# Kernel optimization log

Hardware: AMD Instinct MI355X
Metric: run time of the kernel (lower is better)

The kernel has to match this reference:

```python
import jax, jax.numpy as jnp
import numpy as np

N = 50000      # num_nodes
E = 800000     # num_edges
C = 2000       # num_communities
F_NODE = 26    # n_demographic + 12
F_EDGE = 8     # num_edge_features
DEM = 14       # n_demographic
EMB = 64       # n_embedding
H2 = 2 * EMB   # 2*n_embedding == mask dim
HID = 128      # n_hidden (== H2 so the per-edge mask applies to both convs)


def setup_inputs() -> dict:
    key = jax.random.key(0)
    ks = jax.random.split(key, 40)
    def W(i, shape):
        return jax.random.normal(ks[i], shape, jnp.float32) * 0.05
    z = lambda d: jnp.zeros((d,), jnp.float32)
    return {
        "x": jax.random.normal(ks[0], (N, F_NODE), jnp.float32),
        "edge_attr": jax.random.uniform(ks[1], (E, F_EDGE), dtype=jnp.float32),
        "W_ee": W(2, (F_EDGE, EMB)), "b_ee": z(EMB),
        "W_e1": W(3, (DEM, EMB)), "b_e1": z(EMB),
        "W_e2": W(4, (12, EMB)), "b_e2": z(EMB),
        "W_e3": W(5, (H2, H2)), "b_e3": z(H2),
        "W_src": W(6, (H2, H2)), "W_dst": W(7, (H2, H2)), "W_ea": W(8, (EMB, H2)), "b_el": z(H2),
        "W_m": W(9, (H2, H2)), "b_m": z(H2),
        "W_n1": W(10, (H2, HID)), "W_r1": W(11, (H2, HID)), "b_c1": z(HID),
        "W_n2": W(12, (HID, HID)), "W_r2": W(13, (HID, HID)), "b_c2": z(HID),
        "W_l1": W(14, (2 * HID, HID)), "b_l1": z(HID),
        "W_l2": W(15, (HID, 1)), "b_l2": z(1),
        "edge_index": jax.random.randint(ks[16], (2, E), 0, N),
        "community": jax.random.randint(ks[17], (N,), 0, C),
        "multi_community_nodes": jax.random.randint(ks[18], (1000,), 0, N),
        "multi_community_index": jax.random.randint(ks[19], (1000,), 0, C),
    }


def _pool(h, community):
    # scatter_mean + scatter_max over communities, concatenated: [C, 2*d]
    sums = jax.ops.segment_sum(h, community, num_segments=C)
    cnt = jax.ops.segment_sum(jnp.ones((h.shape[0], 1), h.dtype), community, num_segments=C)
    mean = sums / jnp.maximum(cnt, 1.0)
    mx = jax.ops.segment_max(h, community, num_segments=C)
    mx = jnp.where(jnp.isfinite(mx), mx, 0.0)  # empty segments -> 0 (torch_scatter fill)
    return jnp.concatenate([mean, mx], axis=1)


def reference(x, edge_attr, W_ee, b_ee, W_e1, b_e1, W_e2, b_e2, W_e3, b_e3,
              W_src, W_dst, W_ea, b_el, W_m, b_m,
              W_n1, W_r1, b_c1, W_n2, W_r2, b_c2,
              W_l1, b_l1, W_l2, b_l2,
              edge_index, community, multi_community_nodes, multi_community_index):
    src, dst = edge_index[0], edge_index[1]
    # edge + node embeddings
    e = jax.nn.relu(edge_attr @ W_ee + b_ee)                      # [E, EMB]
    x1 = jax.nn.relu(x[:, :DEM] @ W_e1 + b_e1)                    # [N, EMB]
    x2 = jax.nn.relu(x[:, DEM:] @ W_e2 + b_e2)                    # [N, EMB]
    h = jax.nn.relu(jnp.concatenate([x1, x2], axis=1) @ W_e3 + b_e3)  # [N, H2]
    # edge learning: per-edge soft mask from endpoint features + edge embedding
    he = jax.nn.relu(h[src] @ W_src + h[dst] @ W_dst + e @ W_ea + b_el)  # [E, H2]
    mask = jax.nn.sigmoid(he @ W_m + b_m)                          # [E, H2]
    # mean-normalized masked message passing (ELConv)
    deg = jax.ops.segment_sum(jnp.ones((E, 1), h.dtype), dst, num_segments=N)
    deg_inv = 1.0 / jnp.maximum(deg, 1.0)                          # [N, 1]
    agg1 = jax.ops.segment_sum(h[src] * mask, dst, num_segments=N) * deg_inv
    h1 = jax.nn.relu(agg1 @ W_n1 + h @ W_r1 + b_c1)                # [N, HID]
    p1 = _pool(h1, community)                                      # [C, 2*HID]
    agg2 = jax.ops.segment_sum(h1[src] * mask, dst, num_segments=N) * deg_inv
    h2 = jax.nn.relu(agg2 @ W_n2 + h1 @ W_r2 + b_c2)               # [N, HID]
    p2 = _pool(h2, community)                                      # [C, 2*HID]
    p = p1 + p2
    out = jax.nn.relu(p @ W_l1 + b_l1)  # dropout skipped (eval mode)
    return (out @ W_l2 + b_l2)[:, 0]    # [C]
```

## Files before the change

### kernel.cpp

```cpp
#include <hip/hip_runtime.h>
#include <cstdint>
#include <cstddef>

#define kN 50000
#define kE 800000
#define kC 2000

using s8v = __attribute__((ext_vector_type(8))) short;
using s4v = __attribute__((ext_vector_type(4))) short;
using f4v = __attribute__((ext_vector_type(4))) float;

__device__ __forceinline__ short f2bf(float x){
  union { float f; unsigned u; } v; v.f = x;
  unsigned r = (v.u + 0x7fffu + ((v.u >> 16) & 1u)) >> 16;
  return (short)r;
}
__device__ __forceinline__ float bf2f(short s){
  union { unsigned u; float f; } v; v.u = ((unsigned)(unsigned short)s) << 16;
  return v.f;
}

__global__ __launch_bounds__(256) void k_hist(const int* __restrict__ dst, int* __restrict__ deg,
                                              const int* __restrict__ community, int* __restrict__ ccnt){
  int i = blockIdx.x*256 + threadIdx.x;
  if (i < kE) atomicAdd(&deg[dst[i]], 1);
  if (i < kN) atomicAdd(&ccnt[community[i]], 1);
}

__global__ __launch_bounds__(1024) void k_scan(const int* __restrict__ deg, int* __restrict__ offs){
  __shared__ int s_wsum[16];
  __shared__ int s_woff[17];
  __shared__ int s_carry;
  int t = threadIdx.x, lane = t & 63, w = t >> 6;
  if (t == 0) s_carry = 0;
  __syncthreads();
  for (int base = 0; base < kN; base += 4096){
    int i = base + t*4;
    int4 v = {0,0,0,0};
    if (i < kN) v = *reinterpret_cast<const int4*>(&deg[i]);
    int s = v.x + v.y + v.z + v.w;
    int x = s;
    #pragma unroll
    for (int off = 1; off < 64; off <<= 1){
      int y = __shfl_up(x, off);
      if (lane >= off) x += y;
    }
    if (lane == 63) s_wsum[w] = x;
    __syncthreads();
    if (t == 0){
      int acc = 0;
      for (int q = 0; q < 16; q++){ s_woff[q] = acc; acc += s_wsum[q]; }
      s_woff[16] = acc;
    }
    __syncthreads();
    if (i < kN){
      int pre = s_carry + s_woff[w] + (x - s);
      int4 o; o.x = pre; o.y = pre + v.x; o.z = pre + v.x + v.y; o.w = pre + v.x + v.y + v.z;
      *reinterpret_cast<int4*>(&offs[i]) = o;
    }
    __syncthreads();
    if (t == 0) s_carry += s_woff[16];
    __syncthreads();
  }
  if (t == 0) offs[kN] = s_carry;
}

__global__ __launch_bounds__(512) void k_scan_c(const int* __restrict__ ccnt, int* __restrict__ coffs){
  __shared__ int s_wsum[8];
  __shared__ int s_woff[9];
  int t = threadIdx.x, lane = t & 63, w = t >> 6;
  int i = t*4;
  int4 v = {0,0,0,0};
  if (i < kC) v = *reinterpret_cast<const int4*>(&ccnt[i]);
  int s = v.x + v.y + v.z + v.w;
  int x = s;
  #pragma unroll
  for (int off = 1; off < 64; off <<= 1){
    int y = __shfl_up(x, off);
    if (lane >= off) x += y;
  }
  if (lane == 63) s_wsum[w] = x;
  __syncthreads();
  if (t == 0){
    int a = 0;
    for (int q = 0; q < 8; q++){ s_woff[q] = a; a += s_wsum[q]; }
    s_woff[8] = a;
  }
  __syncthreads();
  if (i < kC){
    int pre = s_woff[w] + (x - s);
    int4 o; o.x = pre; o.y = pre + v.x; o.z = pre + v.x + v.y; o.w = pre + v.x + v.y + v.z;
    *reinterpret_cast<int4*>(&coffs[i]) = o;
  }
  if (t == 0) coffs[kC] = s_woff[8];
}

__global__ __launch_bounds__(256) void k_place(const int* __restrict__ src, const int* __restrict__ dst,
                                               const int* __restrict__ offs, int* __restrict__ cursor,
                                               int* __restrict__ pos_of_edge, int* __restrict__ src_sorted){
  int e = blockIdx.x*256 + threadIdx.x;
  if (e >= kE) return;
  int d = dst[e];
  int p = offs[d] + atomicAdd(&cursor[d], 1);
  pos_of_edge[e] = p;
  src_sorted[p]  = src[e];
}

__global__ __launch_bounds__(256) void k_place_c(const int* __restrict__ community, const int* __restrict__ coffs,
                                                 int* __restrict__ ccursor, int* __restrict__ node_by_comm){
  int n = blockIdx.x*256 + threadIdx.x;
  if (n >= kN) return;
  int c = community[n];
  int p = coffs[c] + atomicAdd(&ccursor[c], 1);
  node_by_comm[p] = n;
}

__global__ __launch_bounds__(512, 2) void k_embed_ab(
    const float* __restrict__ x,
    const float* __restrict__ W_e1, const float* __restrict__ b_e1,
    const float* __restrict__ W_e2, const float* __restrict__ b_e2,
    const float* __restrict__ W_e3, const float* __restrict__ b_e3,
    const float* __restrict__ W_src, const float* __restrict__ W_dst, const float* __restrict__ b_el,
    short* __restrict__ Hout, short* __restrict__ Aout, short* __restrict__ Bout, int ntiles)
{
  __shared__ short s_W[2][128][136];
  __shared__ float s_x[64][28];
  __shared__ float s_b3[128], s_bel[128];
  int tid = threadIdx.x;
  int lane = tid & 63, w = tid >> 6, lo = lane & 15, hi = lane >> 4;
  for (int idx = tid; idx < 128*128; idx += 512){
    int f = idx & 127, k = idx >> 7;
    s_W[0][f][k] = f2bf(W_e3[k*128 + f]);
    s_W[1][f][k] = f2bf(W_src[k*128 + f]);
  }
  if (tid < 128){ s_b3[tid] = b_e3[tid]; s_bel[tid] = b_el[tid]; }
  __syncthreads();
  s8v fe3[4], fsrc[4], fdst[4];
  #pragma unroll
  for (int ks = 0; ks < 4; ks++){
    fe3[ks]  = *(const s8v*)&s_W[0][w*16 + lo][ks*32 + hi*8];
    fsrc[ks] = *(const s8v*)&s_W[1][w*16 + lo][ks*32 + hi*8];
  }
  __syncthreads();
  for (int idx = tid; idx < 128*128; idx += 512){
    int f = idx & 127, k = idx >> 7;
    s_W[0][f][k] = f2bf(W_dst[k*128 + f]);
  }
  __syncthreads();
  #pragma unroll
  for (int ks = 0; ks < 4; ks++) fdst[ks] = *(const s8v*)&s_W[0][w*16 + lo][ks*32 + hi*8];

  short (*s_xe)[136] = s_W[0];
  short (*s_h)[136]  = s_W[1];

  for (int tile = blockIdx.x; tile < ntiles; tile += gridDim.x){
    int n0 = tile << 6;
    __syncthreads();
    for (int idx = tid; idx < 64*26; idx += 512){
      int nl = idx / 26, i = idx - nl*26; int n = n0 + nl;
      s_x[nl][i] = (n < kN) ? x[(size_t)n*26 + i] : 0.f;
    }
    __syncthreads();
    #pragma unroll
    for (int r = 0; r < 16; r++){
      int idx = (r << 9) + tid; int nl = idx >> 7, j = idx & 127;
      float a;
      if (j < 64){
        a = b_e1[j];
        #pragma unroll
        for (int i = 0; i < 14; i++) a += s_x[nl][i] * W_e1[i*64 + j];
      } else {
        int jj = j - 64;
        a = b_e2[jj];
        #pragma unroll
        for (int i = 0; i < 12; i++) a += s_x[nl][14 + i] * W_e2[i*64 + jj];
      }
      s_xe[nl][j] = f2bf(fmaxf(a, 0.f));
    }
    __syncthreads();
    #pragma unroll
    for (int et = 0; et < 4; et++){
      f4v acc = {0.f,0.f,0.f,0.f};
      #pragma unroll
      for (int ks = 0; ks < 4; ks++){
        s8v b = *(const s8v*)&s_xe[et*16 + lo][ks*32 + hi*8];
        acc = __builtin_amdgcn_mfma_f32_16x16x32_bf16(fe3[ks], b, acc, 0, 0, 0);
      }
      int n = n0 + et*16 + lo, f0 = w*16 + hi*4;
      s4v hv;
      #pragma unroll
      for (int j = 0; j < 4; j++) hv[j] = f2bf(fmaxf(acc[j] + s_b3[f0 + j], 0.f));
      *(s4v*)&s_h[et*16 + lo][f0] = hv;
      if (n < kN) *(s4v*)&Hout[(size_t)n*128 + f0] = hv;
    }
    __syncthreads();
    #pragma unroll
    for (int et = 0; et < 4; et++){
      f4v aA = {0.f,0.f,0.f,0.f}, aB = {0.f,0.f,0.f,0.f};
      #pragma unroll
      for (int ks = 0; ks < 4; ks++){
        s8v b = *(const s8v*)&s_h[et*16 + lo][ks*32 + hi*8];
        aA = __builtin_amdgcn_mfma_f32_16x16x32_bf16(fsrc[ks], b, aA, 0, 0, 0);
        aB = __builtin_amdgcn_mfma_f32_16x16x32_bf16(fdst[ks], b, aB, 0, 0, 0);
      }
      int n = n0 + et*16 + lo, f0 = w*16 + hi*4;
      if (n < kN){
        s4v Av, Bv;
        #pragma unroll
        for (int j = 0; j < 4; j++){ Av[j] = f2bf(aA[j] + s_bel[f0 + j]); Bv[j] = f2bf(aB[j]); }
        *(s4v*)&Aout[(size_t)n*128 + f0] = Av;
        *(s4v*)&Bout[(size_t)n*128 + f0] = Bv;
      }
    }
  }
}

#define OFF_WEA  0
#define OFF_WM   18432
#define OFF_EEMB 0
#define OFF_HE   9216
#define OFF_BIAS 26624
#define OFF_EA   59648
#define OFF_WEE  61696
#define OFF_BEE  63744
#define OFF_BM   64000
#define OFF_SRC  64512
#define OFF_DST  64768
#define OFF_POS  65024
__global__ __launch_bounds__(512, 4) void k_edge(
    const short* __restrict__ Abf, const short* __restrict__ Bbf,
    const float* __restrict__ edge_attr,
    const int* __restrict__ src, const int* __restrict__ dst,
    const int* __restrict__ posp,
    const float* __restrict__ W_ee, const float* __restrict__ b_ee,
    const float* __restrict__ W_ea, const float* __restrict__ W_m,
    const float* __restrict__ b_m,
    unsigned char* __restrict__ mask_out,
    int ntiles)
{
  __shared__ __align__(16) char smem[65280];
  short (*s_WeaT)[72]  = (short(*)[72])(smem + OFF_WEA);
  short (*s_WmT)[136]  = (short(*)[136])(smem + OFF_WM);
  short (*s_eemb)[72]  = (short(*)[72])(smem + OFF_EEMB);
  short (*s_he)[136]   = (short(*)[136])(smem + OFF_HE);
  float (*s_bias)[129] = (float(*)[129])(smem + OFF_BIAS);
  float (*s_ea)[8]     = (float(*)[8])(smem + OFF_EA);
  float *s_Wee = (float*)(smem + OFF_WEE);
  float *s_bee = (float*)(smem + OFF_BEE);
  float *s_bm  = (float*)(smem + OFF_BM);
  int *s_src = (int*)(smem + OFF_SRC);
  int *s_dst = (int*)(smem + OFF_DST);
  int *s_pos = (int*)(smem + OFF_POS);

  int tid = threadIdx.x;
  for (int idx = tid; idx < 128*64; idx += 512){ int f = idx & 127, k = idx >> 7; s_WeaT[f][k] = f2bf(W_ea[k*128+f]); }
  for (int idx = tid; idx < 128*128; idx += 512){ int f = idx & 127, k = idx >> 7; s_WmT[f][k] = f2bf(W_m[k*128+f]); }
  s_Wee[tid] = W_ee[tid];
  if (tid < 64) s_bee[tid] = b_ee[tid];
  if (tid >= 64 && tid < 192) s_bm[tid-64] = b_m[tid-64];
  __syncthreads();
  const int lane = tid & 63, w = tid >> 6;
  const int lo = lane & 15, hi = lane >> 4;
  const int el8 = tid >> 3, kb = (tid & 7) << 3;
  s8v a1[2], a2[4];
  #pragma unroll
  for (int ks = 0; ks < 2; ks++) a1[ks] = *(const s8v*)&s_WeaT[16*w + lo][ks*32 + hi*8];
  #pragma unroll
  for (int ks = 0; ks < 4; ks++) a2[ks] = *(const s8v*)&s_WmT[16*w + lo][ks*32 + hi*8];
  __syncthreads();

  for (int tile = blockIdx.x; tile < ntiles; tile += gridDim.x){
    int e0 = tile << 6;
    {
      int el = tid >> 3, i = tid & 7;
      s_ea[el][i] = edge_attr[(size_t)(e0 + el)*8 + i];
      if (tid < 192){
        int q = tid >> 6, r = tid & 63; int ee = e0 + r;
        if (q == 0)      s_src[r] = src[ee];
        else if (q == 1) s_dst[r] = dst[ee];
        else             s_pos[r] = posp[ee];
      }
    }
    __syncthreads();
    {
      int e = el8, part = tid & 7;
      int sb = s_src[e]*128 + part*16;
      int db = s_dst[e]*128 + part*16;
      s8v av0 = *(const s8v*)(Abf + sb);
      s8v av1 = *(const s8v*)(Abf + sb + 8);
      s8v bv0 = *(const s8v*)(Bbf + db);
      s8v bv1 = *(const s8v*)(Bbf + db + 8);
      float ee_[8];
      #pragma unroll
      for (int j = 0; j < 8; j++){
        float acc = s_bee[kb + j];
        #pragma unroll
        for (int i = 0; i < 8; i++) acc += s_ea[e][i] * s_Wee[i*64 + kb + j];
        ee_[j] = fmaxf(acc, 0.f);
      }
      s8v ep;
      #pragma unroll
      for (int j = 0; j < 8; j++) ep[j] = f2bf(ee_[j]);
      *(s8v*)&s_eemb[e][kb] = ep;
      #pragma unroll
      for (int q = 0; q < 8; q++){
        s_bias[e][part*16 + q]     = bf2f(av0[q]) + bf2f(bv0[q]);
        s_bias[e][part*16 + 8 + q] = bf2f(av1[q]) + bf2f(bv1[q]);
      }
    }
    __syncthreads();
    #pragma unroll
    for (int et = 0; et < 4; et++){
      f4v acc = {0.f, 0.f, 0.f, 0.f};
      #pragma unroll
      for (int ks = 0; ks < 2; ks++){
        s8v bfrag = *(const s8v*)&s_eemb[et*16 + lo][ks*32 + hi*8];
        acc = __builtin_amdgcn_mfma_f32_16x16x32_bf16(a1[ks], bfrag, acc, 0, 0, 0);
      }
      int e = et*16 + lo, f0 = 16*w + hi*4;
      s4v hw;
      #pragma unroll
      for (int j = 0; j < 4; j++) hw[j] = f2bf(fmaxf(acc[j] + s_bias[e][f0 + j], 0.f));
      *(s4v*)&s_he[e][f0] = hw;
    }
    __syncthreads();
    #pragma unroll
    for (int et = 0; et < 4; et++){
      f4v acc = {0.f, 0.f, 0.f, 0.f};
      #pragma unroll
      for (int ks = 0; ks < 4; ks++){
        s8v bfrag = *(const s8v*)&s_he[et*16 + lo][ks*32 + hi*8];
        acc = __builtin_amdgcn_mfma_f32_16x16x32_bf16(a2[ks], bfrag, acc, 0, 0, 0);
      }
      int e = et*16 + lo, f0 = 16*w + hi*4;
      unsigned pk = 0;
      #pragma unroll
      for (int j = 0; j < 4; j++){
        float m = 1.f/(1.f + __expf(-(acc[j] + s_bm[f0 + j])));
        pk |= (__float2uint_rn(m*255.f) & 255u) << (j*8);
      }
      *reinterpret_cast<unsigned*>(&mask_out[(size_t)s_pos[e]*128 + f0]) = pk;
    }
    __syncthreads();
  }
}

__global__ __launch_bounds__(512, 8) void k_conv(
    const short* __restrict__ Hbf,
    const unsigned char* __restrict__ mask8,
    const int* __restrict__ src_sorted, const int* __restrict__ offs,
    const float* __restrict__ Wn, const float* __restrict__ Wr, const float* __restrict__ bc,
    short* __restrict__ Hout, float* __restrict__ Pout, int ntiles)
{
  __shared__ short s_buf[128][136];
  __shared__ float s_bc[128];
  int tid = threadIdx.x;
  int lane = tid & 63, w = tid >> 6, lo = lane & 15, hi = lane >> 4;
  s8v fn[4], fr[4];
  for (int idx = tid; idx < 128*128; idx += 512){
    int f = idx & 127, k = idx >> 7;
    s_buf[f][k] = f2bf(Wn[k*128 + f]);
  }
  if (tid < 128) s_bc[tid] = bc[tid];
  __syncthreads();
  #pragma unroll
  for (int ks = 0; ks < 4; ks++) fn[ks] = *(const s8v*)&s_buf[w*16 + lo][ks*32 + hi*8];
  __syncthreads();
  for (int idx = tid; idx < 128*128; idx += 512){
    int f = idx & 127, k = idx >> 7;
    s_buf[f][k] = f2bf(Wr[k*128 + f]);
  }
  __syncthreads();
  #pragma unroll
  for (int ks = 0; ks < 4; ks++) fr[ks] = *(const s8v*)&s_buf[w*16 + lo][ks*32 + hi*8];

  short (*s_agg)[136] = s_buf;
  short (*s_h)[136]   = s_buf + 64;
  const int nl8 = tid >> 3, p16 = (tid & 7) << 4;

  for (int tile = blockIdx.x; tile < ntiles; tile += gridDim.x){
    int n0 = tile << 6;
    __syncthreads();
    int n = n0 + nl8;
    {
      s8v h0 = {0,0,0,0,0,0,0,0}, h1 = {0,0,0,0,0,0,0,0};
      if (n < kN){
        h0 = *(const s8v*)&Hbf[(size_t)n*128 + p16];
        h1 = *(const s8v*)&Hbf[(size_t)n*128 + p16 + 8];
      }
      *(s8v*)&s_h[nl8][p16] = h0;
      *(s8v*)&s_h[nl8][p16 + 8] = h1;
    }
    float acc[16];
    #pragma unroll
    for (int q = 0; q < 16; q++) acc[q] = 0.f;
    int s0 = 0, s1 = 0;
    if (n < kN){ s0 = offs[n]; s1 = offs[n+1]; }
    int4 mv_c = {0,0,0,0}; s8v g0_c = {0,0,0,0,0,0,0,0}, g1_c = {0,0,0,0,0,0,0,0};
    if (s0 < s1){
      int sv = src_sorted[s0];
      mv_c = *reinterpret_cast<const int4*>(&mask8[(size_t)s0*128 + p16]);
      g0_c = *(const s8v*)&Hbf[(size_t)sv*128 + p16];
      g1_c = *(const s8v*)&Hbf[(size_t)sv*128 + p16 + 8];
    }
    for (int i = s0; i < s1; i++){
      int4 mv = mv_c; s8v g0 = g0_c, g1 = g1_c;
      if (i + 1 < s1){
        int svn = src_sorted[i + 1];
        mv_c = *reinterpret_cast<const int4*>(&mask8[(size_t)(i+1)*128 + p16]);
        g0_c = *(const s8v*)&Hbf[(size_t)svn*128 + p16];
        g1_c = *(const s8v*)&Hbf[(size_t)svn*128 + p16 + 8];
      }
      unsigned mw[4] = {(unsigned)mv.x, (unsigned)mv.y, (unsigned)mv.z, (unsigned)mv.w};
      float mf[16];
      #pragma unroll
      for (int d = 0; d < 4; d++){
        mf[d*4+0] = (float)( mw[d]        & 255u);
        mf[d*4+1] = (float)((mw[d] >>  8) & 255u);
        mf[d*4+2] = (float)((mw[d] >> 16) & 255u);
        mf[d*4+3] = (float)( mw[d] >> 24       );
      }
      #pragma unroll
      for (int q = 0; q < 8; q++) acc[q]     += bf2f(g0[q]) * mf[q];
      #pragma unroll
      for (int q = 0; q < 8; q++) acc[8 + q] += bf2f(g1[q]) * mf[8 + q];
    }
    float inv = (1.f/255.f) / fmaxf((float)(s1 - s0), 1.f);
    {
      s8v a0, a1;
      #pragma unroll
      for (int q = 0; q < 8; q++){ a0[q] = f2bf(acc[q]*inv); a1[q] = f2bf(acc[8+q]*inv); }
      *(s8v*)&s_agg[nl8][p16] = a0;
      *(s8v*)&s_agg[nl8][p16 + 8] = a1;
    }
    __syncthreads();
    #pragma unroll
    for (int et = 0; et < 4; et++){
      f4v ac = {0.f,0.f,0.f,0.f};
      #pragma unroll
      for (int ks = 0; ks < 4; ks++){
        s8v bA = *(const s8v*)&s_agg[et*16 + lo][ks*32 + hi*8];
        ac = __builtin_amdgcn_mfma_f32_16x16x32_bf16(fn[ks], bA, ac, 0, 0, 0);
        s8v bH = *(const s8v*)&s_h[et*16 + lo][ks*32 + hi*8];
        ac = __builtin_amdgcn_mfma_f32_16x16x32_bf16(fr[ks], bH, ac, 0, 0, 0);
      }
      int nn = n0 + et*16 + lo, f0 = w*16 + hi*4;
      if (nn < kN){
        s4v hv; float4 pv;
        float v0 = fmaxf(ac[0] + s_bc[f0 + 0], 0.f);
        float v1 = fmaxf(ac[1] + s_bc[f0 + 1], 0.f);
        float v2 = fmaxf(ac[2] + s_bc[f0 + 2], 0.f);
        float v3 = fmaxf(ac[3] + s_bc[f0 + 3], 0.f);
        hv[0] = f2bf(v0); hv[1] = f2bf(v1); hv[2] = f2bf(v2); hv[3] = f2bf(v3);
        pv.x = v0; pv.y = v1; pv.z = v2; pv.w = v3;
        if (Hout) *(s4v*)&Hout[(size_t)nn*128 + f0] = hv;
        *reinterpret_cast<float4*>(&Pout[(size_t)nn*128 + f0]) = pv;
      }
    }
  }
}

__global__ __launch_bounds__(128) void k_final(
    const float* __restrict__ p1f, const float* __restrict__ p2f,
    const int* __restrict__ node_by_comm, const int* __restrict__ coffs,
    const float* __restrict__ W_l1, const float* __restrict__ b_l1,
    const float* __restrict__ W_l2, const float* __restrict__ b_l2,
    float* __restrict__ out)
{
  __shared__ float p[256];
  __shared__ float red[2];
  int c = blockIdx.x, t = threadIdx.x;
  int c0 = coffs[c], c1 = coffs[c+1];
  float s = 0.f, m1 = 0.f, m2 = 0.f;
  float v1_c = 0.f, v2_c = 0.f;
  if (c0 < c1){
    int n = node_by_comm[c0];
    v1_c = p1f[(size_t)n*128 + t];
    v2_c = p2f[(size_t)n*128 + t];
  }
  for (int i = c0; i < c1; i++){
    float v1 = v1_c, v2 = v2_c;
    if (i + 1 < c1){
      int nn = node_by_comm[i + 1];
      v1_c = p1f[(size_t)nn*128 + t];
      v2_c = p2f[(size_t)nn*128 + t];
    }
    s += v1 + v2;
    m1 = fmaxf(m1, v1);
    m2 = fmaxf(m2, v2);
  }
  float inv = 1.f / fmaxf((float)(c1 - c0), 1.f);
  p[t]       = s * inv;
  p[128 + t] = m1 + m2;
  __syncthreads();
  float acc = b_l1[t];
  for (int g = 0; g < 256; g++) acc += p[g]*W_l1[g*128+t];
  float hv = fmaxf(acc, 0.f) * W_l2[t];
  #pragma unroll
  for (int off = 32; off > 0; off >>= 1) hv += __shfl_down(hv, off);
  if ((t & 63) == 0) red[t>>6] = hv;
  __syncthreads();
  if (t == 0) out[c] = red[0] + red[1] + b_l2[0];
}

__global__ void k_diag(float* out, float v){
  int i = blockIdx.x*256 + threadIdx.x;
  if (i < kC) out[i] = v;
}

extern "C" void kernel_launch(void* const* d_in, const int* in_sizes, int n_in,
                              void* d_out, int out_size, void* d_ws, size_t ws_size,
                              hipStream_t stream)
{
  const float* x    = (const float*)d_in[0];
  const float* ea   = (const float*)d_in[1];
  const float* W_ee = (const float*)d_in[2];  const float* b_ee = (const float*)d_in[3];
  const float* W_e1 = (const float*)d_in[4];  const float* b_e1 = (const float*)d_in[5];
  const float* W_e2 = (const float*)d_in[6];  const float* b_e2 = (const float*)d_in[7];
  const float* W_e3 = (const float*)d_in[8];  const float* b_e3 = (const float*)d_in[9];
  const float* W_src= (const float*)d_in[10]; const float* W_dst= (const float*)d_in[11];
  const float* W_ea = (const float*)d_in[12]; const float* b_el = (const float*)d_in[13];
  const float* W_m  = (const float*)d_in[14]; const float* b_m  = (const float*)d_in[15];
  const float* W_n1 = (const float*)d_in[16]; const float* W_r1 = (const float*)d_in[17]; const float* b_c1 = (const float*)d_in[18];
  const float* W_n2 = (const float*)d_in[19]; const float* W_r2 = (const float*)d_in[20]; const float* b_c2 = (const float*)d_in[21];
  const float* W_l1 = (const float*)d_in[22]; const float* b_l1 = (const float*)d_in[23];
  const float* W_l2 = (const float*)d_in[24]; const float* b_l2 = (const float*)d_in[25];
  const int* eidx   = (const int*)d_in[26];
  const int* srcp   = eidx;
  const int* dstp   = eidx + kE;
  const int* community = (const int*)d_in[27];
  float* out = (float*)d_out;

  char* ws = (char*)d_ws;
  size_t off = 0;
  auto take = [&](size_t bytes)->char*{
    char* p = ws + off;
    off += (bytes + 511) & ~(size_t)511;
    return p;
  };
  const size_t NB2 = (size_t)kN*128*2;
  const size_t NB4 = (size_t)kN*128*4;
  short* hbuf  = (short*)take(NB2);
  short* h1buf = (short*)take(NB2);
  short* Abf16 = (short*)take(NB2);
  short* Bbf16 = (short*)take(NB2);
  float* p1f   = (float*)take(NB4);
  float* p2f   = (float*)take(NB4);
  char* z0 = ws + off;
  int* deg     = (int*)take((size_t)kN*4);
  int* cursor  = (int*)take((size_t)kN*4);
  int* ccnt    = (int*)take((size_t)kC*4);
  int* ccursor = (int*)take((size_t)kC*4);
  size_t zbytes = (size_t)((ws + off) - z0);
  int* offs    = (int*)take((size_t)(kN+1)*4);
  int* coffs   = (int*)take((size_t)(kC+1)*4);
  int* node_by_comm = (int*)take((size_t)kN*4);
  unsigned char* mask8 = (unsigned char*)take((size_t)kE*128);
  int* src_sorted  = (int*)take((size_t)kE*4);
  int* pos_of_edge = (int*)take((size_t)kE*4);
  size_t need = off;

  const int ntE   = (kE + 63) / 64;
  const int ntN64 = (kN + 63) / 64;

  if (ws_size >= need){
    hipMemsetAsync(z0, 0, zbytes, stream);
    k_hist    <<<(kE+255)/256, 256, 0, stream>>>(dstp, deg, community, ccnt);
    k_embed_ab<<<512, 512, 0, stream>>>(x, W_e1,b_e1, W_e2,b_e2, W_e3,b_e3,
                                        W_src, W_dst, b_el, hbuf, Abf16, Bbf16, ntN64);
    k_scan    <<<1, 1024, 0, stream>>>(deg, offs);
    k_scan_c  <<<1, 512, 0, stream>>>(ccnt, coffs);
    k_place   <<<(kE+255)/256, 256, 0, stream>>>(srcp, dstp, offs, cursor, pos_of_edge, src_sorted);
    k_place_c <<<(kN+255)/256, 256, 0, stream>>>(community, coffs, ccursor, node_by_comm);
    k_edge    <<<512, 512, 0, stream>>>(Abf16, Bbf16, ea, srcp, dstp, pos_of_edge,
                                        W_ee, b_ee, W_ea, W_m, b_m, mask8, ntE);
    k_conv    <<<ntN64, 512, 0, stream>>>(hbuf, mask8, src_sorted, offs,
                                          W_n1, W_r1, b_c1, h1buf, p1f, ntN64);
    k_conv    <<<ntN64, 512, 0, stream>>>(h1buf, mask8, src_sorted, offs,
                                          W_n2, W_r2, b_c2, nullptr, p2f, ntN64);
    k_final   <<<kC, 128, 0, stream>>>(p1f, p2f, node_by_comm, coffs,
                                       W_l1, b_l1, W_l2, b_l2, out);
  } else {
    k_diag<<<8, 256, 0, stream>>>(out, (float)(ws_size >> 20));
  }
}
```

Measured before the change: 514.1 us.

## Shrink k_edge LDS by gathering endpoint bias into MFMA accumulators

The per-edge endpoint features A[src]+B[dst] are now loaded directly in the MFMA output layout and used as the initial accumulator, which removes the large fp32 s_bias shared-memory tile. Weight fragments are staged through a reused scratch region, so LDS drops from about 64KB to about 34KB. That allows launch bounds of 8 blocks and a grid of 1024 blocks, raising occupancy. f2bf now uses the HIP intrinsic. The trade-off is narrower 8-byte scattered gathers per lane and more registers held across the tile loop.

```diff
diff --git a/kernel.cpp b/kernel.cpp
--- a/kernel.cpp
+++ b/kernel.cpp
@@ -1,4 +1,5 @@
 #include <hip/hip_runtime.h>
+#include <hip/hip_bf16.h>
 #include <cstdint>
 #include <cstddef>
 
@@ -11,9 +12,8 @@
 using f4v = __attribute__((ext_vector_type(4))) float;
 
 __device__ __forceinline__ short f2bf(float x){
-  union { float f; unsigned u; } v; v.f = x;
-  unsigned r = (v.u + 0x7fffu + ((v.u >> 16) & 1u)) >> 16;
-  return (short)r;
+  __hip_bfloat16 h = __float2bfloat16(x);
+  return *reinterpret_cast<short*>(&h);
 }
 __device__ __forceinline__ float bf2f(short s){
   union { unsigned u; float f; } v; v.u = ((unsigned)(unsigned short)s) << 16;
@@ -215,19 +215,17 @@
   }
 }
 
-#define OFF_WEA  0
-#define OFF_WM   18432
-#define OFF_EEMB 0
-#define OFF_HE   9216
-#define OFF_BIAS 26624
-#define OFF_EA   59648
-#define OFF_WEE  61696
-#define OFF_BEE  63744
-#define OFF_BM   64000
-#define OFF_SRC  64512
-#define OFF_DST  64768
-#define OFF_POS  65024
-__global__ __launch_bounds__(512, 4) void k_edge(
+#define KE_LDS  34816
+#define RO_EEMB 0
+#define RO_HE   9216
+#define RO_EA   26624
+#define RO_WEE  28672
+#define RO_BEE  30720
+#define RO_BM   30976
+#define RO_SRC  31488
+#define RO_DST  31744
+#define RO_POS  32000
+__global__ __launch_bounds__(512, 8) void k_edge(
     const short* __restrict__ Abf, const short* __restrict__ Bbf,
     const float* __restrict__ edge_attr,
     const int* __restrict__ src, const int* __restrict__ dst,
@@ -238,36 +236,44 @@
     unsigned char* __restrict__ mask_out,
     int ntiles)
 {
-  __shared__ __align__(16) char smem[65280];
-  short (*s_WeaT)[72]  = (short(*)[72])(smem + OFF_WEA);
-  short (*s_WmT)[136]  = (short(*)[136])(smem + OFF_WM);
-  short (*s_eemb)[72]  = (short(*)[72])(smem + OFF_EEMB);
-  short (*s_he)[136]   = (short(*)[136])(smem + OFF_HE);
-  float (*s_bias)[129] = (float(*)[129])(smem + OFF_BIAS);
-  float (*s_ea)[8]     = (float(*)[8])(smem + OFF_EA);
-  float *s_Wee = (float*)(smem + OFF_WEE);
-  float *s_bee = (float*)(smem + OFF_BEE);
-  float *s_bm  = (float*)(smem + OFF_BM);
-  int *s_src = (int*)(smem + OFF_SRC);
-  int *s_dst = (int*)(smem + OFF_DST);
-  int *s_pos = (int*)(smem + OFF_POS);
+  __shared__ __align__(16) char smem[KE_LDS];
+  short (*s_eemb)[72]  = (short(*)[72])(smem + RO_EEMB);
+  short (*s_he)[136]   = (short(*)[136])(smem + RO_HE);
+  float (*s_ea)[8]     = (float(*)[8])(smem + RO_EA);
+  float *s_Wee = (float*)(smem + RO_WEE);
+  float *s_bee = (float*)(smem + RO_BEE);
+  float *s_bm  = (float*)(smem + RO_BM);
+  int *s_src = (int*)(smem + RO_SRC);
+  int *s_dst = (int*)(smem + RO_DST);
+  int *s_pos = (int*)(smem + RO_POS);
 
   int tid = threadIdx.x;
-  for (int idx = tid; idx < 128*64; idx += 512){ int f = idx & 127, k = idx >> 7; s_WeaT[f][k] = f2bf(W_ea[k*128+f]); }
-  for (int idx = tid; idx < 128*128; idx += 512){ int f = idx & 127, k = idx >> 7; s_WmT[f][k] = f2bf(W_m[k*128+f]); }
+  const int lane = tid & 63, w = tid >> 6;
+  const int lo = lane & 15, hi = lane >> 4;
+
+  s8v a1[2], a2[4];
+  {
+    short (*s_stg)[72] = (short(*)[72])smem;
+    for (int idx = tid; idx < 128*64; idx += 512){ int f = idx & 127, k = idx >> 7; s_stg[f][k] = f2bf(W_ea[k*128+f]); }
+    __syncthreads();
+    #pragma unroll
+    for (int ks = 0; ks < 2; ks++) a1[ks] = *(const s8v*)&s_stg[16*w + lo][ks*32 + hi*8];
+    __syncthreads();
+  }
+  {
+    short (*s_stg)[136] = (short(*)[136])smem;
+    for (int idx = tid; idx < 128*128; idx += 512){ int f = idx & 127, k = idx >> 7; s_stg[f][k] = f2bf(W_m[k*128+f]); }
+    __syncthreads();
+    #pragma unroll
+    for (int ks = 0; ks < 4; ks++) a2[ks] = *(const s8v*)&s_stg[16*w + lo][ks*32 + hi*8];
+    __syncthreads();
+  }
   s_Wee[tid] = W_ee[tid];
   if (tid < 64) s_bee[tid] = b_ee[tid];
   if (tid >= 64 && tid < 192) s_bm[tid-64] = b_m[tid-64];
-  __syncthreads();
-  const int lane = tid & 63, w = tid >> 6;
-  const int lo = lane & 15, hi = lane >> 4;
+
   const int el8 = tid >> 3, kb = (tid & 7) << 3;
-  s8v a1[2], a2[4];
-  #pragma unroll
-  for (int ks = 0; ks < 2; ks++) a1[ks] = *(const s8v*)&s_WeaT[16*w + lo][ks*32 + hi*8];
-  #pragma unroll
-  for (int ks = 0; ks < 4; ks++) a2[ks] = *(const s8v*)&s_WmT[16*w + lo][ks*32 + hi*8];
-  __syncthreads();
+  const int f0 = 16*w + hi*4;
 
   for (int tile = blockIdx.x; tile < ntiles; tile += gridDim.x){
     int e0 = tile << 6;
@@ -282,46 +288,44 @@
       }
     }
     __syncthreads();
+    s4v av[4], bv[4]; int pr[4];
+    #pragma unroll
+    for (int et = 0; et < 4; et++){
+      int e = et*16 + lo;
+      int sr = s_src[e], dr = s_dst[e];
+      pr[et] = s_pos[e];
+      av[et] = *(const s4v*)(Abf + (size_t)sr*128 + f0);
+      bv[et] = *(const s4v*)(Bbf + (size_t)dr*128 + f0);
+    }
     {
-      int e = el8, part = tid & 7;
-      int sb = s_src[e]*128 + part*16;
-      int db = s_dst[e]*128 + part*16;
-      s8v av0 = *(const s8v*)(Abf + sb);
-      s8v av1 = *(const s8v*)(Abf + sb + 8);
-      s8v bv0 = *(const s8v*)(Bbf + db);
-      s8v bv1 = *(const s8v*)(Bbf + db + 8);
       float ee_[8];
       #pragma unroll
       for (int j = 0; j < 8; j++){
         float acc = s_bee[kb + j];
         #pragma unroll
-        for (int i = 0; i < 8; i++) acc += s_ea[e][i] * s_Wee[i*64 + kb + j];
+        for (int i = 0; i < 8; i++) acc += s_ea[el8][i] * s_Wee[i*64 + kb + j];
         ee_[j] = fmaxf(acc, 0.f);
       }
       s8v ep;
       #pragma unroll
       for (int j = 0; j < 8; j++) ep[j] = f2bf(ee_[j]);
-      *(s8v*)&s_eemb[e][kb] = ep;
-      #pragma unroll
-      for (int q = 0; q < 8; q++){
-        s_bias[e][part*16 + q]     = bf2f(av0[q]) + bf2f(bv0[q]);
-        s_bias[e][part*16 + 8 + q] = bf2f(av1[q]) + bf2f(bv1[q]);
-      }
+      *(s8v*)&s_eemb[el8][kb] = ep;
     }
     __syncthreads();
     #pragma unroll
     for (int et = 0; et < 4; et++){
-      f4v acc = {0.f, 0.f, 0.f, 0.f};
+      f4v acc;
+      #pragma unroll
+      for (int j = 0; j < 4; j++) acc[j] = bf2f(av[et][j]) + bf2f(bv[et][j]);
       #pragma unroll
       for (int ks = 0; ks < 2; ks++){
         s8v bfrag = *(const s8v*)&s_eemb[et*16 + lo][ks*32 + hi*8];
         acc = __builtin_amdgcn_mfma_f32_16x16x32_bf16(a1[ks], bfrag, acc, 0, 0, 0);
       }
-      int e = et*16 + lo, f0 = 16*w + hi*4;
       s4v hw;
       #pragma unroll
-      for (int j = 0; j < 4; j++) hw[j] = f2bf(fmaxf(acc[j] + s_bias[e][f0 + j], 0.f));
-      *(s4v*)&s_he[e][f0] = hw;
+      for (int j = 0; j < 4; j++) hw[j] = f2bf(fmaxf(acc[j], 0.f));
+      *(s4v*)&s_he[et*16 + lo][f0] = hw;
     }
     __syncthreads();
     #pragma unroll
@@ -332,14 +336,13 @@
         s8v bfrag = *(const s8v*)&s_he[et*16 + lo][ks*32 + hi*8];
         acc = __builtin_amdgcn_mfma_f32_16x16x32_bf16(a2[ks], bfrag, acc, 0, 0, 0);
       }
-      int e = et*16 + lo, f0 = 16*w + hi*4;
       unsigned pk = 0;
       #pragma unroll
       for (int j = 0; j < 4; j++){
         float m = 1.f/(1.f + __expf(-(acc[j] + s_bm[f0 + j])));
         pk |= (__float2uint_rn(m*255.f) & 255u) << (j*8);
       }
-      *reinterpret_cast<unsigned*>(&mask_out[(size_t)s_pos[e]*128 + f0]) = pk;
+      *reinterpret_cast<unsigned*>(&mask_out[(size_t)pr[et]*128 + f0]) = pk;
     }
     __syncthreads();
   }
@@ -572,8 +575,8 @@
     k_scan_c  <<<1, 512, 0, stream>>>(ccnt, coffs);
     k_place   <<<(kE+255)/256, 256, 0, stream>>>(srcp, dstp, offs, cursor, pos_of_edge, src_sorted);
     k_place_c <<<(kN+255)/256, 256, 0, stream>>>(community, coffs, ccursor, node_by_comm);
-    k_edge    <<<512, 512, 0, stream>>>(Abf16, Bbf16, ea, srcp, dstp, pos_of_edge,
-                                        W_ee, b_ee, W_ea, W_m, b_m, mask8, ntE);
+    k_edge    <<<1024, 512, 0, stream>>>(Abf16, Bbf16, ea, srcp, dstp, pos_of_edge,
+                                         W_ee, b_ee, W_ea, W_m, b_m, mask8, ntE);
     k_conv    <<<ntN64, 512, 0, stream>>>(hbuf, mask8, src_sorted, offs,
                                           W_n1, W_r1, b_c1, h1buf, p1f, ntN64);
     k_conv    <<<ntN64, 512, 0, stream>>>(h1buf, mask8, src_sorted, offs,
```

After: 836.5 us. 1.63x slower.
